# Optimization experiments

Measured on AMD Instinct MI355X. Metric: run time of the kernel, lower is better.

## Reference

```python
import jax, jax.numpy as jnp
import numpy as np
from jax import lax

# dims: batch, seq len, views, d_model; d_state, d_inner=2*d_model, d_conv, dt_rank=ceil(d_model/16)
B, L, V, D = 4, 512, 4, 256
DS, DI, DCONV, DTR = 16, 512, 4, 16
EPS = 1e-5

def setup_inputs():
    key = jax.random.key(0)
    ks = jax.random.split(key, 10)
    rn = lambda k, s, sc: jax.random.normal(k, s, jnp.float32) * sc
    return {
        "x": rn(ks[0], (B, L, V, D), 1.0),
        "ln_g": jnp.ones((V, D), jnp.float32),
        "ln_b": jnp.zeros((V, D), jnp.float32),
        "w_in": rn(ks[1], (V, 2 * DI, D), D ** -0.5),
        "conv_w": rn(ks[2], (V, DI, DCONV), DCONV ** -0.5),
        "conv_b": rn(ks[3], (V, DI), 0.02),
        "w_x": rn(ks[4], (V, DTR + 2 * DS, DI), DI ** -0.5),
        "w_dt": rn(ks[5], (V, DI, DTR), DTR ** -0.5),
        "b_dt": rn(ks[6], (V, DI), 0.02),
        "A_log": rn(ks[7], (V, DI, DS), 0.5),
        "D_skip": jnp.ones((V, DI), jnp.float32),
        "w_out": rn(ks[8], (V, D, DI), DI ** -0.5),
    }

def _layernorm(x, g, b):
    mu = x.mean(-1, keepdims=True)
    var = ((x - mu) ** 2).mean(-1, keepdims=True)
    return (x - mu) * lax.rsqrt(var + EPS) * g + b

def _mamba_view(xv, w_in, conv_w, conv_b, w_x, w_dt, b_dt, A_log, D_skip, w_out):
    # xv: (B, L, D)
    xz = jnp.einsum('bld,ed->ble', xv, w_in)            # (B, L, 2*DI)
    xi, z = xz[..., :DI], xz[..., DI:]
    # causal depthwise conv over time
    xt = jnp.moveaxis(xi, 1, 2)                          # (B, DI, L)
    xt = jnp.pad(xt, ((0, 0), (0, 0), (DCONV - 1, 0)))
    xc = lax.conv_general_dilated(xt, conv_w[:, None, :], (1,), 'VALID',
                                  feature_group_count=DI,
                                  dimension_numbers=('NCH', 'OIH', 'NCH'))
    xc = jax.nn.silu(xc + conv_b[None, :, None])
    xc = jnp.moveaxis(xc, 1, 2)                          # (B, L, DI)
    xdbl = jnp.einsum('bld,ed->ble', xc, w_x)            # (B, L, DTR+2*DS)
    dt_lo = xdbl[..., :DTR]
    Bc = xdbl[..., DTR:DTR + DS]
    Cc = xdbl[..., DTR + DS:]
    delta = jax.nn.softplus(jnp.einsum('blr,dr->bld', dt_lo, w_dt) + b_dt)
    A = -jnp.exp(A_log)                                  # (DI, DS)
    dA = jnp.exp(jnp.einsum('bld,dn->bldn', delta, A))   # discretized A
    dBu = jnp.einsum('bld,bln,bld->bldn', delta, Bc, xc) # discretized B*u

    def step(h, inp):
        dA_t, dBu_t, C_t = inp
        h = dA_t * h + dBu_t                             # (B, DI, DS)
        return h, jnp.einsum('bdn,bn->bd', h, C_t)

    h0 = jnp.zeros((B, DI, DS), xv.dtype)
    _, ys = lax.scan(step, h0, (jnp.moveaxis(dA, 1, 0), jnp.moveaxis(dBu, 1, 0), jnp.moveaxis(Cc, 1, 0)))
    y = jnp.moveaxis(ys, 0, 1) + xc * D_skip             # (B, L, DI)
    y = y * jax.nn.silu(z)
    return jnp.einsum('bld,od->blo', y, w_out)           # (B, L, D)

def _forward(x, ln_g, ln_b, w_in, conv_w, conv_b, w_x, w_dt, b_dt, A_log, D_skip, w_out):
    xv = jnp.moveaxis(x, 2, 0)                           # (V, B, L, D)
    def per_view(xv_i, g, b, wi, cw, cb, wx, wdt, bdt, al, dsk, wo):
        return _mamba_view(_layernorm(xv_i, g, b), wi, cw, cb, wx, wdt, bdt, al, dsk, wo)
    outs = jax.vmap(per_view)(xv, ln_g, ln_b, w_in, conv_w, conv_b, w_x, w_dt, b_dt, A_log, D_skip, w_out)
    return jnp.moveaxis(outs, 0, 2)                      # (B, L, V, D)

def reference(x, ln_g, ln_b, w_in, conv_w, conv_b, w_x, w_dt, b_dt, A_log, D_skip, w_out):
    # eval mode: view_mask == ones, dropout identity, gather is None -> h == agents
    agents = _forward(x, ln_g, ln_b, w_in, conv_w, conv_b, w_x, w_dt, b_dt, A_log, D_skip, w_out)
    return (agents, agents)
```

## Files before the change

### kernel.cpp

```cpp
#include <hip/hip_runtime.h>
#include <hip/hip_bf16.h>
#include <math.h>

#define B_ 4
#define L_ 512
#define V_ 4
#define D_ 256
#define DS_ 16
#define DI_ 512
#define DTR_ 16
#define ML (B_*L_)
#define NC_ 32
#define CL_ 16

#define OFF_RA   0
#define SZ_RA    ((long)V_*ML*D_)
#define OFF_XZ   (OFF_RA + SZ_RA)
#define SZ_XZ    ((long)V_*ML*2*DI_)
#define OFF_XC   (OFF_XZ + SZ_XZ)
#define SZ_XC    ((long)V_*ML*DI_)
#define OFF_XDBL (OFF_XC + SZ_XC)
#define SZ_XDBL  ((long)V_*ML*48)

typedef short short8_t __attribute__((ext_vector_type(8)));
typedef float f32x4_t  __attribute__((ext_vector_type(4)));

#define LOG2E 1.44269504088896341f
#define LN2   0.69314718055994531f

__device__ __forceinline__ float exp2_fast(float x) { return __builtin_amdgcn_exp2f(x); }
__device__ __forceinline__ float softplus_fast(float x) {
    const float t = __builtin_amdgcn_exp2f(x * LOG2E);
    const float r = __builtin_amdgcn_logf(1.f + t) * LN2;
    return x > 20.f ? x : r;
}
__device__ __forceinline__ float silu_fast(float z) {
    const float t = __builtin_amdgcn_exp2f(-LOG2E * z);
    return z * __builtin_amdgcn_rcpf(1.f + t);
}
__device__ __forceinline__ ushort f2bf(float f) {
    uint u = __float_as_uint(f);
    return (ushort)((u + 0x7fffu + ((u >> 16) & 1u)) >> 16);
}
__device__ __forceinline__ float bf2f(ushort h) { return __uint_as_float(((uint)h) << 16); }

__device__ __forceinline__ long hb_idx(int v, int b, int c, int d) {
    const long s = ((((long)b*NC_ + c)*DI_ + d) << 4);
    return (long)v*ML*(2*DI_) + (s >> 9)*(2*DI_) + (s & 511);
}

__global__ __launch_bounds__(256) void split_w(const float* __restrict__ in,
                                               ushort* __restrict__ oh,
                                               ushort* __restrict__ ol, int n4)
{
    const int i = blockIdx.x*256 + threadIdx.x;
    if (i >= n4) return;
    const float4 f = ((const float4*)in)[i];
    const ushort h0=f2bf(f.x), h1=f2bf(f.y), h2=f2bf(f.z), h3=f2bf(f.w);
    ((short4*)oh)[i] = make_short4((short)h0,(short)h1,(short)h2,(short)h3);
    ((short4*)ol)[i] = make_short4((short)f2bf(f.x-bf2f(h0)), (short)f2bf(f.y-bf2f(h1)),
                                   (short)f2bf(f.z-bf2f(h2)), (short)f2bf(f.w-bf2f(h3)));
}

__global__ __launch_bounds__(256) void ln_split(const float* __restrict__ x,
                                                const float* __restrict__ g,
                                                const float* __restrict__ bta,
                                                ushort* __restrict__ xh,
                                                ushort* __restrict__ xl)
{
    const int m = blockIdx.x;
    const int v = blockIdx.y;
    const int d = threadIdx.x;
    const float val = x[((long)m*V_ + v)*D_ + d];
    float s = val, sq = val*val;
#pragma unroll
    for (int off = 32; off >= 1; off >>= 1) {
        s  += __shfl_xor(s, off);
        sq += __shfl_xor(sq, off);
    }
    __shared__ float ws[4], wq[4];
    if ((threadIdx.x & 63) == 0) { ws[threadIdx.x >> 6] = s; wq[threadIdx.x >> 6] = sq; }
    __syncthreads();
    s  = ws[0]+ws[1]+ws[2]+ws[3];
    sq = wq[0]+wq[1]+wq[2]+wq[3];
    const float mu  = s * (1.f/D_);
    const float var = sq * (1.f/D_) - mu*mu;
    const float inv = rsqrtf(var + 1e-5f);
    const float r = (val - mu)*inv*g[v*D_+d] + bta[v*D_+d];
    const ushort h = f2bf(r);
    const long idx = ((long)v*ML + m)*D_ + d;
    xh[idx] = h;
    xl[idx] = f2bf(r - bf2f(h));
}

__global__ __launch_bounds__(256,2) void mfma_gemm_in(
    const ushort* __restrict__ Ah, const ushort* __restrict__ Al,
    const ushort* __restrict__ Bh, const ushort* __restrict__ Bl,
    float* __restrict__ C)
{
    const int v = blockIdx.z;
    const long Ao = (long)v*ML*D_;
    const long Bo = (long)v*(2*DI_)*D_;
    C += (long)v*ML*(2*DI_);
    const int bm = blockIdx.y*128, bn = blockIdx.x*128;
    __shared__ ushort sAh[128][40], sAl[128][40], sBh[128][40], sBl[128][40];
    const int tid  = threadIdx.x;
    const int lane = tid & 63, w = tid >> 6;
    const int wr = w >> 1, wc = w & 1;
    const int fm = lane & 15, fg = lane >> 4;
    const int r = tid >> 1, q0 = (tid & 1)*2;

    f32x4_t acc[4][4];
#pragma unroll
    for (int i=0;i<4;++i)
#pragma unroll
        for (int j=0;j<4;++j)
#pragma unroll
            for (int k=0;k<4;++k) acc[i][j][k]=0.f;

    const ushort* Agh = Ah + Ao + (long)(bm+r)*D_ + q0*8;
    const ushort* Agl = Al + Ao + (long)(bm+r)*D_ + q0*8;
    const ushort* Bgh = Bh + Bo + (long)(bn+r)*D_ + q0*8;
    const ushort* Bgl = Bl + Bo + (long)(bn+r)*D_ + q0*8;

    for (int k0 = 0; k0 < D_; k0 += 32) {
        const uint4 a0 = *(const uint4*)(Agh + k0);
        const uint4 a1 = *(const uint4*)(Agh + k0 + 8);
        const uint4 a2 = *(const uint4*)(Agl + k0);
        const uint4 a3 = *(const uint4*)(Agl + k0 + 8);
        const uint4 b0 = *(const uint4*)(Bgh + k0);
        const uint4 b1 = *(const uint4*)(Bgh + k0 + 8);
        const uint4 b2 = *(const uint4*)(Bgl + k0);
        const uint4 b3 = *(const uint4*)(Bgl + k0 + 8);
        __syncthreads();
        *(uint4*)&sAh[r][q0*8]   = a0;  *(uint4*)&sAh[r][q0*8+8] = a1;
        *(uint4*)&sAl[r][q0*8]   = a2;  *(uint4*)&sAl[r][q0*8+8] = a3;
        *(uint4*)&sBh[r][q0*8]   = b0;  *(uint4*)&sBh[r][q0*8+8] = b1;
        *(uint4*)&sBl[r][q0*8]   = b2;  *(uint4*)&sBl[r][q0*8+8] = b3;
        __syncthreads();
        short8_t ah[4], al[4], bh[4], bl[4];
#pragma unroll
        for (int i=0;i<4;++i) {
            ah[i] = *(const short8_t*)&sAh[wr*64 + i*16 + fm][fg*8];
            al[i] = *(const short8_t*)&sAl[wr*64 + i*16 + fm][fg*8];
            bh[i] = *(const short8_t*)&sBh[wc*64 + i*16 + fm][fg*8];
            bl[i] = *(const short8_t*)&sBl[wc*64 + i*16 + fm][fg*8];
        }
#pragma unroll
        for (int i=0;i<4;++i)
#pragma unroll
            for (int j=0;j<4;++j) {
                acc[i][j] = __builtin_amdgcn_mfma_f32_16x16x32_bf16(ah[i], bh[j], acc[i][j], 0,0,0);
                acc[i][j] = __builtin_amdgcn_mfma_f32_16x16x32_bf16(ah[i], bl[j], acc[i][j], 0,0,0);
                acc[i][j] = __builtin_amdgcn_mfma_f32_16x16x32_bf16(al[i], bh[j], acc[i][j], 0,0,0);
            }
    }
#pragma unroll
    for (int i=0;i<4;++i)
#pragma unroll
        for (int j4=0;j4<4;++j4) {
            const int row = bm + wr*64 + i*16 + fg*4 + j4;
            float* cr = C + (long)row*(2*DI_) + bn + wc*64 + fm;
#pragma unroll
            for (int j=0;j<4;++j) cr[j*16] = acc[i][j][j4];
        }
}

__global__ __launch_bounds__(256,2) void mfma_gemm_out(
    const uint* __restrict__ Apk,
    const ushort* __restrict__ Bh, const ushort* __restrict__ Bl,
    float* __restrict__ Cout)
{
    const int v = blockIdx.z;
    Apk += (long)v*ML*DI_;
    const long Bo = (long)v*D_*DI_;
    const int bm = blockIdx.y*128, bn = blockIdx.x*128;
    __shared__ ushort sAh[128][40], sAl[128][40], sBh[128][40], sBl[128][40];
    const int tid  = threadIdx.x;
    const int lane = tid & 63, w = tid >> 6;
    const int wr = w >> 1, wc = w & 1;
    const int fm = lane & 15, fg = lane >> 4;
    const int r = tid >> 1, hh = tid & 1, q0 = (tid & 1)*2;

    f32x4_t acc[4][4];
#pragma unroll
    for (int i=0;i<4;++i)
#pragma unroll
        for (int j=0;j<4;++j)
#pragma unroll
            for (int k=0;k<4;++k) acc[i][j][k]=0.f;

    const uint*   Ag  = Apk + (long)(bm+r)*DI_ + hh*16;
    const ushort* Bgh = Bh + Bo + (long)(bn+r)*DI_ + q0*8;
    const ushort* Bgl = Bl + Bo + (long)(bn+r)*DI_ + q0*8;

    for (int k0 = 0; k0 < DI_; k0 += 32) {
        const uint4 p0 = *(const uint4*)(Ag + k0);
        const uint4 p1 = *(const uint4*)(Ag + k0 + 4);
        const uint4 p2 = *(const uint4*)(Ag + k0 + 8);
        const uint4 p3 = *(const uint4*)(Ag + k0 + 12);
        const uint4 b0 = *(const uint4*)(Bgh + k0);
        const uint4 b1 = *(const uint4*)(Bgh + k0 + 8);
        const uint4 b2 = *(const uint4*)(Bgl + k0);
        const uint4 b3 = *(const uint4*)(Bgl + k0 + 8);
        __syncthreads();
        *(short4*)&sAh[r][hh*16+ 0] = make_short4((short)(p0.x&0xffff),(short)(p0.y&0xffff),(short)(p0.z&0xffff),(short)(p0.w&0xffff));
        *(short4*)&sAl[r][hh*16+ 0] = make_short4((short)(p0.x>>16),(short)(p0.y>>16),(short)(p0.z>>16),(short)(p0.w>>16));
        *(short4*)&sAh[r][hh*16+ 4] = make_short4((short)(p1.x&0xffff),(short)(p1.y&0xffff),(short)(p1.z&0xffff),(short)(p1.w&0xffff));
        *(short4*)&sAl[r][hh*16+ 4] = make_short4((short)(p1.x>>16),(short)(p1.y>>16),(short)(p1.z>>16),(short)(p1.w>>16));
        *(short4*)&sAh[r][hh*16+ 8] = make_short4((short)(p2.x&0xffff),(short)(p2.y&0xffff),(short)(p2.z&0xffff),(short)(p2.w&0xffff));
        *(short4*)&sAl[r][hh*16+ 8] = make_short4((short)(p2.x>>16),(short)(p2.y>>16),(short)(p2.z>>16),(short)(p2.w>>16));
        *(short4*)&sAh[r][hh*16+12] = make_short4((short)(p3.x&0xffff),(short)(p3.y&0xffff),(short)(p3.z&0xffff),(short)(p3.w&0xffff));
        *(short4*)&sAl[r][hh*16+12] = make_short4((short)(p3.x>>16),(short)(p3.y>>16),(short)(p3.z>>16),(short)(p3.w>>16));
        *(uint4*)&sBh[r][q0*8]   = b0;  *(uint4*)&sBh[r][q0*8+8] = b1;
        *(uint4*)&sBl[r][q0*8]   = b2;  *(uint4*)&sBl[r][q0*8+8] = b3;
        __syncthreads();
        short8_t ah[4], al[4], bh[4], bl[4];
#pragma unroll
        for (int i=0;i<4;++i) {
            ah[i] = *(const short8_t*)&sAh[wr*64 + i*16 + fm][fg*8];
            al[i] = *(const short8_t*)&sAl[wr*64 + i*16 + fm][fg*8];
            bh[i] = *(const short8_t*)&sBh[wc*64 + i*16 + fm][fg*8];
            bl[i] = *(const short8_t*)&sBl[wc*64 + i*16 + fm][fg*8];
        }
#pragma unroll
        for (int i=0;i<4;++i)
#pragma unroll
            for (int j=0;j<4;++j) {
                acc[i][j] = __builtin_amdgcn_mfma_f32_16x16x32_bf16(ah[i], bh[j], acc[i][j], 0,0,0);
                acc[i][j] = __builtin_amdgcn_mfma_f32_16x16x32_bf16(ah[i], bl[j], acc[i][j], 0,0,0);
                acc[i][j] = __builtin_amdgcn_mfma_f32_16x16x32_bf16(al[i], bh[j], acc[i][j], 0,0,0);
            }
    }
    const long TOT = (long)ML * V_ * D_;
#pragma unroll
    for (int i=0;i<4;++i)
#pragma unroll
        for (int j4=0;j4<4;++j4) {
            const int row = bm + wr*64 + i*16 + fg*4 + j4;
#pragma unroll
            for (int j=0;j<4;++j) {
                const int col = bn + wc*64 + j*16 + fm;
                const long base = ((long)row*V_ + v)*D_ + col;
                const float val = acc[i][j][j4];
                Cout[base]       = val;
                Cout[base + TOT] = val;
            }
        }
}

__global__ __launch_bounds__(512) void conv_silu(const float* __restrict__ xz,
                                                 const float* __restrict__ cw,
                                                 const float* __restrict__ cb,
                                                 float* __restrict__ xc)
{
    const int m = blockIdx.x;
    const int v = blockIdx.y;
    const int c = threadIdx.x;
    const int l = m & 511;
    const float* xzv = xz + (long)v*ML*2*DI_;
    const float4 w4 = *(const float4*)&cw[((long)v*DI_ + c)*4];
    const float w[4] = {w4.x, w4.y, w4.z, w4.w};
    float acc = cb[v*DI_ + c];
#pragma unroll
    for (int k = 0; k < 4; ++k) {
        const int lp = l - 3 + k;
        if (lp >= 0) acc = fmaf(xzv[(long)(m - 3 + k)*(2*DI_) + c], w[k], acc);
    }
    xc[((long)v*ML + m)*DI_ + c] = silu_fast(acc);
}

__global__ __launch_bounds__(256) void gemm_nt48_sk(const float* __restrict__ A,
                                                    const float* __restrict__ Bm,
                                                    float* __restrict__ P,
                                                    long sAv, long sBv)
{
    const int v = blockIdx.z;
    const int ks = blockIdx.y;
    A  += (long)v * sAv;
    Bm += (long)v * sBv;
    P  += (long)v * ((long)ML*2*DI_);
    __shared__ float As[16][68];
    __shared__ float Bs[16][48];
    const int tid = threadIdx.x;
    const int tx = tid & 15, ty = tid >> 4;
    const int bm = blockIdx.x * 64;
    const int lr = tid >> 2;
    const int lk = (tid & 3) * 4;
    const float* Ag = A + (long)(bm + lr)*DI_ + lk;
    float acc[4][3] = {};
    for (int k0 = ks*128; k0 < ks*128 + 128; k0 += 16) {
        const float4 av = *(const float4*)(Ag + k0);
        float4 bv = {0,0,0,0};
        if (tid < 192) bv = *(const float4*)(Bm + (long)(tid >> 2)*DI_ + k0 + (tid & 3)*4);
        __syncthreads();
        As[lk+0][lr]=av.x; As[lk+1][lr]=av.y; As[lk+2][lr]=av.z; As[lk+3][lr]=av.w;
        if (tid < 192) {
            const int br = tid >> 2, bk = (tid & 3)*4;
            Bs[bk+0][br]=bv.x; Bs[bk+1][br]=bv.y; Bs[bk+2][br]=bv.z; Bs[bk+3][br]=bv.w;
        }
        __syncthreads();
#pragma unroll
        for (int kk = 0; kk < 16; ++kk) {
            const float4 a = *(const float4*)&As[kk][ty*4];
            const float b0 = Bs[kk][tx*3+0], b1 = Bs[kk][tx*3+1], b2 = Bs[kk][tx*3+2];
            acc[0][0]=fmaf(a.x,b0,acc[0][0]); acc[0][1]=fmaf(a.x,b1,acc[0][1]); acc[0][2]=fmaf(a.x,b2,acc[0][2]);
            acc[1][0]=fmaf(a.y,b0,acc[1][0]); acc[1][1]=fmaf(a.y,b1,acc[1][1]); acc[1][2]=fmaf(a.y,b2,acc[1][2]);
            acc[2][0]=fmaf(a.z,b0,acc[2][0]); acc[2][1]=fmaf(a.z,b1,acc[2][1]); acc[2][2]=fmaf(a.z,b2,acc[2][2]);
            acc[3][0]=fmaf(a.w,b0,acc[3][0]); acc[3][1]=fmaf(a.w,b1,acc[3][1]); acc[3][2]=fmaf(a.w,b2,acc[3][2]);
        }
    }
#pragma unroll
    for (int i = 0; i < 4; ++i)
#pragma unroll
        for (int j = 0; j < 3; ++j)
            P[(long)(bm + ty*4 + i)*(2*DI_) + ks*48 + tx*3 + j] = acc[i][j];
}

__global__ __launch_bounds__(256) void reduce48(const float* __restrict__ xz,
                                                float* __restrict__ xdbl)
{
    const long i = (long)blockIdx.x*256 + threadIdx.x;
    if (i >= (long)V_*ML*48) return;
    const long row = i / 48; const int j = (int)(i % 48);
    const float* p = xz + row*(2*DI_);
    xdbl[i] = (p[j] + p[48+j]) + (p[96+j] + p[144+j]);
}

__global__ __launch_bounds__(256) void scanA(const float* __restrict__ xcin,
                                             const float* __restrict__ xdbl,
                                             const float* __restrict__ A_log,
                                             const float* __restrict__ wdt,
                                             const float* __restrict__ bdt,
                                             float* __restrict__ hxz,
                                             float* __restrict__ sdel)
{
    const int c = blockIdx.x >> 1, half = blockIdx.x & 1;
    const int b = blockIdx.y, v = blockIdx.z;
    const int d = half*256 + threadIdx.x;
    const long rowbase = (long)v*ML + (long)b*L_ + (long)c*CL_;
    const float* xcv = xcin + rowbase*DI_;
    const float* xdv = xdbl + rowbase*48;

    __shared__ float sX[CL_*48];
    for (int t = threadIdx.x; t < CL_*48; t += 256) sX[t] = xdv[t];

    float a2[16];
#pragma unroll
    for (int n = 0; n < 16; ++n)
        a2[n] = -exp2_fast(A_log[((long)v*DI_ + d)*DS_ + n] * LOG2E) * LOG2E;
    float wreg[16];
    {
        const float* wp = wdt + ((long)v*DI_ + d)*DTR_;
#pragma unroll
        for (int r = 0; r < 16; r += 4) {
            const float4 t4 = *(const float4*)(wp + r);
            wreg[r]=t4.x; wreg[r+1]=t4.y; wreg[r+2]=t4.z; wreg[r+3]=t4.w;
        }
    }
    const float bias = bdt[(long)v*DI_ + d];
    float h[16];
#pragma unroll
    for (int n = 0; n < 16; ++n) h[n] = 0.f;
    float sdsum = 0.f;
    __syncthreads();

    float xcur[8], xnxt[8];
#pragma unroll
    for (int s = 0; s < 8; ++s) xcur[s] = xcv[(long)s*DI_ + d];

    for (int g = 0; g < CL_; g += 8) {
        if (g + 8 < CL_) {
#pragma unroll
            for (int s = 0; s < 8; ++s) xnxt[s] = xcv[(long)(g+8+s)*DI_ + d];
        }
#pragma unroll
        for (int s = 0; s < 8; ++s) {
            const float* xrow = &sX[(g+s)*48];
            const float4 t0 = *(const float4*)&xrow[0];
            const float4 t1 = *(const float4*)&xrow[4];
            const float4 t2 = *(const float4*)&xrow[8];
            const float4 t3 = *(const float4*)&xrow[12];
            float acc = bias;
            acc = fmaf(t0.x,wreg[0],acc);  acc = fmaf(t0.y,wreg[1],acc);
            acc = fmaf(t0.z,wreg[2],acc);  acc = fmaf(t0.w,wreg[3],acc);
            acc = fmaf(t1.x,wreg[4],acc);  acc = fmaf(t1.y,wreg[5],acc);
            acc = fmaf(t1.z,wreg[6],acc);  acc = fmaf(t1.w,wreg[7],acc);
            acc = fmaf(t2.x,wreg[8],acc);  acc = fmaf(t2.y,wreg[9],acc);
            acc = fmaf(t2.z,wreg[10],acc); acc = fmaf(t2.w,wreg[11],acc);
            acc = fmaf(t3.x,wreg[12],acc); acc = fmaf(t3.y,wreg[13],acc);
            acc = fmaf(t3.z,wreg[14],acc); acc = fmaf(t3.w,wreg[15],acc);
            const float delta = softplus_fast(acc);
            const float tx = delta * xcur[s];
            sdsum += delta;
#pragma unroll
            for (int n4 = 0; n4 < 4; ++n4) {
                const float4 Bv = *(const float4*)&xrow[16 + n4*4];
                h[n4*4+0] = fmaf(exp2_fast(delta*a2[n4*4+0]), h[n4*4+0], tx*Bv.x);
                h[n4*4+1] = fmaf(exp2_fast(delta*a2[n4*4+1]), h[n4*4+1], tx*Bv.y);
                h[n4*4+2] = fmaf(exp2_fast(delta*a2[n4*4+2]), h[n4*4+2], tx*Bv.z);
                h[n4*4+3] = fmaf(exp2_fast(delta*a2[n4*4+3]), h[n4*4+3], tx*Bv.w);
            }
        }
#pragma unroll
        for (int s = 0; s < 8; ++s) xcur[s] = xnxt[s];
    }
    float* hb = hxz + hb_idx(v, b, c, d);
#pragma unroll
    for (int n = 0; n < 16; n += 4) {
        float4 r; r.x = h[n]; r.y = h[n+1]; r.z = h[n+2]; r.w = h[n+3];
        *(float4*)&hb[n] = r;
    }
    sdel[(((long)v*B_ + b)*NC_ + c)*DI_ + d] = sdsum;
}

__global__ __launch_bounds__(256) void scanB(const float* __restrict__ A_log,
                                             const float* __restrict__ sdel,
                                             float* __restrict__ hxz)
{
    const long lin = (long)blockIdx.x*256 + threadIdx.x;
    const int n = (int)(lin & 15);
    const int d = (int)((lin >> 4) & 511);
    const int b = (int)((lin >> 13) & 3);
    const int v = (int)(lin >> 15);
    const float a2 = -exp2_fast(A_log[((long)v*DI_ + d)*DS_ + n] * LOG2E) * LOG2E;
    float h = 0.f;
    long hidx = hb_idx(v, b, 0, d) + n;
    long sidx = ((long)(v*B_ + b)*NC_)*DI_ + d;
#pragma unroll
    for (int c = 0; c < NC_; ++c) {
        const float he = hxz[hidx];
        const float P  = exp2_fast(a2 * sdel[sidx]);
        hxz[hidx] = h;
        h = fmaf(P, h, he);
        hidx += (long)16*(2*DI_);
        sidx += DI_;
    }
}

__global__ __launch_bounds__(256) void scanC(const float* __restrict__ xz,
                                             const float* __restrict__ xcin,
                                             const float* __restrict__ xdbl,
                                             const float* __restrict__ A_log,
                                             const float* __restrict__ wdt,
                                             const float* __restrict__ bdt,
                                             const float* __restrict__ D_skip,
                                             float* __restrict__ yout)
{
    const int c = blockIdx.x >> 1, half = blockIdx.x & 1;
    const int b = blockIdx.y, v = blockIdx.z;
    const int d = half*256 + threadIdx.x;
    const long rowbase = (long)v*ML + (long)b*L_ + (long)c*CL_;
    const float* xzv = xz   + rowbase*(2*DI_);
    const float* xcv = xcin + rowbase*DI_;
    const float* xdv = xdbl + rowbase*48;
    uint*        yv  = (uint*)yout + rowbase*DI_;

    __shared__ float sX[CL_*48];
    for (int t = threadIdx.x; t < CL_*48; t += 256) sX[t] = xdv[t];

    float a2[16];
#pragma unroll
    for (int n = 0; n < 16; ++n)
        a2[n] = -exp2_fast(A_log[((long)v*DI_ + d)*DS_ + n] * LOG2E) * LOG2E;
    float wreg[16];
    {
        const float* wp = wdt + ((long)v*DI_ + d)*DTR_;
#pragma unroll
        for (int r = 0; r < 16; r += 4) {
            const float4 t4 = *(const float4*)(wp + r);
            wreg[r]=t4.x; wreg[r+1]=t4.y; wreg[r+2]=t4.z; wreg[r+3]=t4.w;
        }
    }
    const float bias = bdt[(long)v*DI_ + d];
    const float dsk = D_skip[v*DI_ + d];
    float h[16];
    const float* hb = xz + hb_idx(v, b, c, d);
#pragma unroll
    for (int n = 0; n < 16; n += 4) {
        const float4 r = *(const float4*)&hb[n];
        h[n] = r.x; h[n+1] = r.y; h[n+2] = r.z; h[n+3] = r.w;
    }
    __syncthreads();

    float xcur[8], zcur[8], xnxt[8], znxt[8];
#pragma unroll
    for (int s = 0; s < 8; ++s) {
        xcur[s] = xcv[(long)s*DI_ + d];
        zcur[s] = xzv[(long)s*(2*DI_) + DI_ + d];
    }

    for (int g = 0; g < CL_; g += 8) {
        if (g + 8 < CL_) {
#pragma unroll
            for (int s = 0; s < 8; ++s) {
                xnxt[s] = xcv[(long)(g+8+s)*DI_ + d];
                znxt[s] = xzv[(long)(g+8+s)*(2*DI_) + DI_ + d];
            }
        }
#pragma unroll
        for (int s = 0; s < 8; ++s) {
            const float* xrow = &sX[(g+s)*48];
            const float4 t0 = *(const float4*)&xrow[0];
            const float4 t1 = *(const float4*)&xrow[4];
            const float4 t2 = *(const float4*)&xrow[8];
            const float4 t3 = *(const float4*)&xrow[12];
            float acc = bias;
            acc = fmaf(t0.x,wreg[0],acc);  acc = fmaf(t0.y,wreg[1],acc);
            acc = fmaf(t0.z,wreg[2],acc);  acc = fmaf(t0.w,wreg[3],acc);
            acc = fmaf(t1.x,wreg[4],acc);  acc = fmaf(t1.y,wreg[5],acc);
            acc = fmaf(t1.z,wreg[6],acc);  acc = fmaf(t1.w,wreg[7],acc);
            acc = fmaf(t2.x,wreg[8],acc);  acc = fmaf(t2.y,wreg[9],acc);
            acc = fmaf(t2.z,wreg[10],acc); acc = fmaf(t2.w,wreg[11],acc);
            acc = fmaf(t3.x,wreg[12],acc); acc = fmaf(t3.y,wreg[13],acc);
            acc = fmaf(t3.z,wreg[14],acc); acc = fmaf(t3.w,wreg[15],acc);
            const float delta = softplus_fast(acc);
            const float xcval = xcur[s];
            const float tx = delta * xcval;
            float ys = 0.f;
#pragma unroll
            for (int n4 = 0; n4 < 4; ++n4) {
                const float4 Bv = *(const float4*)&xrow[16 + n4*4];
                const float4 Cv = *(const float4*)&xrow[32 + n4*4];
                h[n4*4+0] = fmaf(exp2_fast(delta*a2[n4*4+0]), h[n4*4+0], tx*Bv.x);
                h[n4*4+1] = fmaf(exp2_fast(delta*a2[n4*4+1]), h[n4*4+1], tx*Bv.y);
                h[n4*4+2] = fmaf(exp2_fast(delta*a2[n4*4+2]), h[n4*4+2], tx*Bv.z);
                h[n4*4+3] = fmaf(exp2_fast(delta*a2[n4*4+3]), h[n4*4+3], tx*Bv.w);
                ys = fmaf(h[n4*4+0], Cv.x, ys);
                ys = fmaf(h[n4*4+1], Cv.y, ys);
                ys = fmaf(h[n4*4+2], Cv.z, ys);
                ys = fmaf(h[n4*4+3], Cv.w, ys);
            }
            float outv = ys + xcval * dsk;
            outv *= silu_fast(zcur[s]);
            const ushort hv = f2bf(outv);
            const ushort lv = f2bf(outv - bf2f(hv));
            yv[(long)(g+s)*DI_ + d] = (uint)hv | ((uint)lv << 16);
        }
#pragma unroll
        for (int s = 0; s < 8; ++s) { xcur[s] = xnxt[s]; zcur[s] = znxt[s]; }
    }
}

extern "C" void kernel_launch(void* const* d_in, const int* in_sizes, int n_in,
                              void* d_out, int out_size, void* d_ws, size_t ws_size,
                              hipStream_t stream)
{
    const float* x      = (const float*)d_in[0];
    const float* ln_g   = (const float*)d_in[1];
    const float* ln_b   = (const float*)d_in[2];
    const float* w_in   = (const float*)d_in[3];
    const float* conv_w = (const float*)d_in[4];
    const float* conv_b = (const float*)d_in[5];
    const float* w_x    = (const float*)d_in[6];
    const float* w_dt   = (const float*)d_in[7];
    const float* b_dt   = (const float*)d_in[8];
    const float* A_log  = (const float*)d_in[9];
    const float* D_skip = (const float*)d_in[10];
    const float* w_out  = (const float*)d_in[11];
    float* out = (float*)d_out;

    float* ws   = (float*)d_ws;
    float* xz   = ws + OFF_XZ;
    float* xc   = ws + OFF_XC;
    float* xdbl = ws + OFF_XDBL;
    float* sdel = ws + OFF_RA;

    ushort* xlnh = (ushort*)(ws + OFF_RA);
    ushort* xlnl = xlnh + (long)V_*ML*D_;
    ushort* wih = (ushort*)(ws + OFF_XC);
    ushort* wil = wih + (long)V_*(2*DI_)*D_;
    ushort* woh = (ushort*)(ws + OFF_RA);
    ushort* wol = woh + (long)V_*D_*DI_;

    split_w<<<dim3((V_*(2*DI_)*D_/4 + 255)/256), 256, 0, stream>>>(w_in, wih, wil, V_*(2*DI_)*D_/4);

    ln_split<<<dim3(ML, V_), 256, 0, stream>>>(x, ln_g, ln_b, xlnh, xlnl);

    mfma_gemm_in<<<dim3((2*DI_)/128, ML/128, V_), 256, 0, stream>>>(xlnh, xlnl, wih, wil, xz);

    conv_silu<<<dim3(ML, V_), DI_, 0, stream>>>(xz, conv_w, conv_b, xc);

    gemm_nt48_sk<<<dim3(ML/64, 4, V_), 256, 0, stream>>>(
        xc, w_x, xz, (long)ML*DI_, (long)48*DI_);
    reduce48<<<dim3((V_*ML*48 + 255)/256), 256, 0, stream>>>(xz, xdbl);

    scanA<<<dim3(NC_*2, B_, V_), 256, 0, stream>>>(xc, xdbl, A_log, w_dt, b_dt, xz, sdel);
    scanB<<<dim3((V_*B_*DI_*DS_)/256), 256, 0, stream>>>(A_log, sdel, xz);
    scanC<<<dim3(NC_*2, B_, V_), 256, 0, stream>>>(xz, xc, xdbl, A_log, w_dt, b_dt,
                                                   D_skip, xc);

    split_w<<<dim3((V_*D_*DI_/4 + 255)/256), 256, 0, stream>>>(w_out, woh, wol, V_*D_*DI_/4);

    mfma_gemm_out<<<dim3(D_/128, ML/128, V_), 256, 0, stream>>>((const uint*)xc, woh, wol, out);
}
```

Measured before the change: 228.2 us.

## Drop LDS staging in MFMA GEMMs, fuse split-K reduction into scan, separate workspace buffers

The input and output MFMA GEMMs now load their bf16 hi/lo fragments straight from global memory into registers instead of staging them through shared memory with barriers. The output GEMM uses 64-row tiles over a separate hi/lo y layout, which doubles its grid. The standalone reduce48 kernel is removed, and scanA/scanC sum the four split-K partials while loading their shared tile. The workspace is split into dedicated, non-aliased buffers and both weight splits run up front. The aim is to cut barrier overhead, one kernel launch and a round trip through memory, at the cost of uncoalesced, non-shared global fragment loads that rely on the cache for reuse across waves.

```diff
diff --git a/kernel.cpp b/kernel.cpp
--- a/kernel.cpp
+++ b/kernel.cpp
@@ -13,14 +13,24 @@
 #define NC_ 32
 #define CL_ 16
 
-#define OFF_RA   0
-#define SZ_RA    ((long)V_*ML*D_)
-#define OFF_XZ   (OFF_RA + SZ_RA)
-#define SZ_XZ    ((long)V_*ML*2*DI_)
-#define OFF_XC   (OFF_XZ + SZ_XZ)
-#define SZ_XC    ((long)V_*ML*DI_)
-#define OFF_XDBL (OFF_XC + SZ_XC)
-#define SZ_XDBL  ((long)V_*ML*48)
+#define OFF_XZ    0L
+#define SZ_XZ     ((long)V_*ML*2*DI_)
+#define OFF_XC    (OFF_XZ + SZ_XZ)
+#define SZ_XC     ((long)V_*ML*DI_)
+#define OFF_XLN   (OFF_XC + SZ_XC)
+#define SZ_XLN    ((long)V_*ML*D_)
+#define OFF_WIN   (OFF_XLN + SZ_XLN)
+#define SZ_WIN    ((long)V_*(2*DI_)*D_)
+#define OFF_WOUT  (OFF_WIN + SZ_WIN)
+#define SZ_WOUT   ((long)V_*D_*DI_)
+#define OFF_Y     (OFF_WOUT + SZ_WOUT)
+#define SZ_Y      ((long)V_*ML*DI_)
+#define OFF_P     (OFF_Y + SZ_Y)
+#define SZ_P      ((long)V_*ML*192)
+#define OFF_HB    (OFF_P + SZ_P)
+#define SZ_HB     ((long)V_*B_*NC_*DI_*16)
+#define OFF_SDEL  (OFF_HB + SZ_HB)
+#define SZ_SDEL   ((long)V_*B_*NC_*DI_)
 
 typedef short short8_t __attribute__((ext_vector_type(8)));
 typedef float f32x4_t  __attribute__((ext_vector_type(4)));
@@ -43,11 +53,6 @@
     return (ushort)((u + 0x7fffu + ((u >> 16) & 1u)) >> 16);
 }
 __device__ __forceinline__ float bf2f(ushort h) { return __uint_as_float(((uint)h) << 16); }
-
-__device__ __forceinline__ long hb_idx(int v, int b, int c, int d) {
-    const long s = ((((long)b*NC_ + c)*DI_ + d) << 4);
-    return (long)v*ML*(2*DI_) + (s >> 9)*(2*DI_) + (s & 511);
-}
 
 __global__ __launch_bounds__(256) void split_w(const float* __restrict__ in,
                                                ushort* __restrict__ oh,
@@ -93,22 +98,19 @@
     xl[idx] = f2bf(r - bf2f(h));
 }
 
-__global__ __launch_bounds__(256,2) void mfma_gemm_in(
+__global__ __launch_bounds__(256) void mfma_gemm_in(
     const ushort* __restrict__ Ah, const ushort* __restrict__ Al,
     const ushort* __restrict__ Bh, const ushort* __restrict__ Bl,
     float* __restrict__ C)
 {
     const int v = blockIdx.z;
-    const long Ao = (long)v*ML*D_;
-    const long Bo = (long)v*(2*DI_)*D_;
-    C += (long)v*ML*(2*DI_);
     const int bm = blockIdx.y*128, bn = blockIdx.x*128;
-    __shared__ ushort sAh[128][40], sAl[128][40], sBh[128][40], sBl[128][40];
-    const int tid  = threadIdx.x;
-    const int lane = tid & 63, w = tid >> 6;
+    const int lane = threadIdx.x & 63, w = threadIdx.x >> 6;
     const int wr = w >> 1, wc = w & 1;
     const int fm = lane & 15, fg = lane >> 4;
-    const int r = tid >> 1, q0 = (tid & 1)*2;
+    const long Ab = (long)v*ML*D_       + (long)(bm + wr*64 + fm)*D_ + fg*8;
+    const long Bb = (long)v*(2*DI_)*D_  + (long)(bn + wc*64 + fm)*D_ + fg*8;
+    C += (long)v*ML*(2*DI_);
 
     f32x4_t acc[4][4];
 #pragma unroll
@@ -118,33 +120,15 @@
 #pragma unroll
             for (int k=0;k<4;++k) acc[i][j][k]=0.f;
 
-    const ushort* Agh = Ah + Ao + (long)(bm+r)*D_ + q0*8;
-    const ushort* Agl = Al + Ao + (long)(bm+r)*D_ + q0*8;
-    const ushort* Bgh = Bh + Bo + (long)(bn+r)*D_ + q0*8;
-    const ushort* Bgl = Bl + Bo + (long)(bn+r)*D_ + q0*8;
-
+#pragma unroll 2
     for (int k0 = 0; k0 < D_; k0 += 32) {
-        const uint4 a0 = *(const uint4*)(Agh + k0);
-        const uint4 a1 = *(const uint4*)(Agh + k0 + 8);
-        const uint4 a2 = *(const uint4*)(Agl + k0);
-        const uint4 a3 = *(const uint4*)(Agl + k0 + 8);
-        const uint4 b0 = *(const uint4*)(Bgh + k0);
-        const uint4 b1 = *(const uint4*)(Bgh + k0 + 8);
-        const uint4 b2 = *(const uint4*)(Bgl + k0);
-        const uint4 b3 = *(const uint4*)(Bgl + k0 + 8);
-        __syncthreads();
-        *(uint4*)&sAh[r][q0*8]   = a0;  *(uint4*)&sAh[r][q0*8+8] = a1;
-        *(uint4*)&sAl[r][q0*8]   = a2;  *(uint4*)&sAl[r][q0*8+8] = a3;
-        *(uint4*)&sBh[r][q0*8]   = b0;  *(uint4*)&sBh[r][q0*8+8] = b1;
-        *(uint4*)&sBl[r][q0*8]   = b2;  *(uint4*)&sBl[r][q0*8+8] = b3;
-        __syncthreads();
         short8_t ah[4], al[4], bh[4], bl[4];
 #pragma unroll
-        for (int i=0;i<4;++i) {
-            ah[i] = *(const short8_t*)&sAh[wr*64 + i*16 + fm][fg*8];
-            al[i] = *(const short8_t*)&sAl[wr*64 + i*16 + fm][fg*8];
-            bh[i] = *(const short8_t*)&sBh[wc*64 + i*16 + fm][fg*8];
-            bl[i] = *(const short8_t*)&sBl[wc*64 + i*16 + fm][fg*8];
+        for (int i = 0; i < 4; ++i) {
+            ah[i] = *(const short8_t*)(Ah + Ab + (long)i*16*D_ + k0);
+            al[i] = *(const short8_t*)(Al + Ab + (long)i*16*D_ + k0);
+            bh[i] = *(const short8_t*)(Bh + Bb + (long)i*16*D_ + k0);
+            bl[i] = *(const short8_t*)(Bl + Bb + (long)i*16*D_ + k0);
         }
 #pragma unroll
         for (int i=0;i<4;++i)
@@ -166,65 +150,42 @@
         }
 }
 
-__global__ __launch_bounds__(256,2) void mfma_gemm_out(
-    const uint* __restrict__ Apk,
-    const ushort* __restrict__ Bh, const ushort* __restrict__ Bl,
+__global__ __launch_bounds__(256) void mfma_gemm_out(
+    const ushort* __restrict__ Ahp, const ushort* __restrict__ Alp,
+    const ushort* __restrict__ Bh,  const ushort* __restrict__ Bl,
     float* __restrict__ Cout)
 {
     const int v = blockIdx.z;
-    Apk += (long)v*ML*DI_;
-    const long Bo = (long)v*D_*DI_;
-    const int bm = blockIdx.y*128, bn = blockIdx.x*128;
-    __shared__ ushort sAh[128][40], sAl[128][40], sBh[128][40], sBl[128][40];
-    const int tid  = threadIdx.x;
-    const int lane = tid & 63, w = tid >> 6;
+    const int bm = blockIdx.y*64, bn = blockIdx.x*128;
+    const int lane = threadIdx.x & 63, w = threadIdx.x >> 6;
     const int wr = w >> 1, wc = w & 1;
     const int fm = lane & 15, fg = lane >> 4;
-    const int r = tid >> 1, hh = tid & 1, q0 = (tid & 1)*2;
-
-    f32x4_t acc[4][4];
-#pragma unroll
-    for (int i=0;i<4;++i)
+    const long Ab = (long)v*ML*DI_ + (long)(bm + wr*32 + fm)*DI_ + fg*8;
+    const long Bb = (long)v*D_*DI_ + (long)(bn + wc*64 + fm)*DI_ + fg*8;
+
+    f32x4_t acc[2][4];
+#pragma unroll
+    for (int i=0;i<2;++i)
 #pragma unroll
         for (int j=0;j<4;++j)
 #pragma unroll
             for (int k=0;k<4;++k) acc[i][j][k]=0.f;
 
-    const uint*   Ag  = Apk + (long)(bm+r)*DI_ + hh*16;
-    const ushort* Bgh = Bh + Bo + (long)(bn+r)*DI_ + q0*8;
-    const ushort* Bgl = Bl + Bo + (long)(bn+r)*DI_ + q0*8;
-
+#pragma unroll 2
     for (int k0 = 0; k0 < DI_; k0 += 32) {
-        const uint4 p0 = *(const uint4*)(Ag + k0);
-        const uint4 p1 = *(const uint4*)(Ag + k0 + 4);
-        const uint4 p2 = *(const uint4*)(Ag + k0 + 8);
-        const uint4 p3 = *(const uint4*)(Ag + k0 + 12);
-        const uint4 b0 = *(const uint4*)(Bgh + k0);
-        const uint4 b1 = *(const uint4*)(Bgh + k0 + 8);
-        const uint4 b2 = *(const uint4*)(Bgl + k0);
-        const uint4 b3 = *(const uint4*)(Bgl + k0 + 8);
-        __syncthreads();
-        *(short4*)&sAh[r][hh*16+ 0] = make_short4((short)(p0.x&0xffff),(short)(p0.y&0xffff),(short)(p0.z&0xffff),(short)(p0.w&0xffff));
-        *(short4*)&sAl[r][hh*16+ 0] = make_short4((short)(p0.x>>16),(short)(p0.y>>16),(short)(p0.z>>16),(short)(p0.w>>16));
-        *(short4*)&sAh[r][hh*16+ 4] = make_short4((short)(p1.x&0xffff),(short)(p1.y&0xffff),(short)(p1.z&0xffff),(short)(p1.w&0xffff));
-        *(short4*)&sAl[r][hh*16+ 4] = make_short4((short)(p1.x>>16),(short)(p1.y>>16),(short)(p1.z>>16),(short)(p1.w>>16));
-        *(short4*)&sAh[r][hh*16+ 8] = make_short4((short)(p2.x&0xffff),(short)(p2.y&0xffff),(short)(p2.z&0xffff),(short)(p2.w&0xffff));
-        *(short4*)&sAl[r][hh*16+ 8] = make_short4((short)(p2.x>>16),(short)(p2.y>>16),(short)(p2.z>>16),(short)(p2.w>>16));
-        *(short4*)&sAh[r][hh*16+12] = make_short4((short)(p3.x&0xffff),(short)(p3.y&0xffff),(short)(p3.z&0xffff),(short)(p3.w&0xffff));
-        *(short4*)&sAl[r][hh*16+12] = make_short4((short)(p3.x>>16),(short)(p3.y>>16),(short)(p3.z>>16),(short)(p3.w>>16));
-        *(uint4*)&sBh[r][q0*8]   = b0;  *(uint4*)&sBh[r][q0*8+8] = b1;
-        *(uint4*)&sBl[r][q0*8]   = b2;  *(uint4*)&sBl[r][q0*8+8] = b3;
-        __syncthreads();
-        short8_t ah[4], al[4], bh[4], bl[4];
-#pragma unroll
-        for (int i=0;i<4;++i) {
-            ah[i] = *(const short8_t*)&sAh[wr*64 + i*16 + fm][fg*8];
-            al[i] = *(const short8_t*)&sAl[wr*64 + i*16 + fm][fg*8];
-            bh[i] = *(const short8_t*)&sBh[wc*64 + i*16 + fm][fg*8];
-            bl[i] = *(const short8_t*)&sBl[wc*64 + i*16 + fm][fg*8];
-        }
-#pragma unroll
-        for (int i=0;i<4;++i)
+        short8_t ah[2], al[2], bh[4], bl[4];
+#pragma unroll
+        for (int i = 0; i < 2; ++i) {
+            ah[i] = *(const short8_t*)(Ahp + Ab + (long)i*16*DI_ + k0);
+            al[i] = *(const short8_t*)(Alp + Ab + (long)i*16*DI_ + k0);
+        }
+#pragma unroll
+        for (int j = 0; j < 4; ++j) {
+            bh[j] = *(const short8_t*)(Bh + Bb + (long)j*16*DI_ + k0);
+            bl[j] = *(const short8_t*)(Bl + Bb + (long)j*16*DI_ + k0);
+        }
+#pragma unroll
+        for (int i=0;i<2;++i)
 #pragma unroll
             for (int j=0;j<4;++j) {
                 acc[i][j] = __builtin_amdgcn_mfma_f32_16x16x32_bf16(ah[i], bh[j], acc[i][j], 0,0,0);
@@ -234,10 +195,10 @@
     }
     const long TOT = (long)ML * V_ * D_;
 #pragma unroll
-    for (int i=0;i<4;++i)
+    for (int i=0;i<2;++i)
 #pragma unroll
         for (int j4=0;j4<4;++j4) {
-            const int row = bm + wr*64 + i*16 + fg*4 + j4;
+            const int row = bm + wr*32 + i*16 + fg*4 + j4;
 #pragma unroll
             for (int j=0;j<4;++j) {
                 const int col = bn + wc*64 + j*16 + fm;
@@ -272,14 +233,13 @@
 
 __global__ __launch_bounds__(256) void gemm_nt48_sk(const float* __restrict__ A,
                                                     const float* __restrict__ Bm,
-                                                    float* __restrict__ P,
-                                                    long sAv, long sBv)
+                                                    float* __restrict__ P)
 {
     const int v = blockIdx.z;
     const int ks = blockIdx.y;
-    A  += (long)v * sAv;
-    Bm += (long)v * sBv;
-    P  += (long)v * ((long)ML*2*DI_);
+    A  += (long)v * ((long)ML*DI_);
+    Bm += (long)v * ((long)48*DI_);
+    P  += (long)v * ((long)ML*192);
     __shared__ float As[16][68];
     __shared__ float Bs[16][48];
     const int tid = threadIdx.x;
@@ -314,25 +274,15 @@
     for (int i = 0; i < 4; ++i)
 #pragma unroll
         for (int j = 0; j < 3; ++j)
-            P[(long)(bm + ty*4 + i)*(2*DI_) + ks*48 + tx*3 + j] = acc[i][j];
-}
-
-__global__ __launch_bounds__(256) void reduce48(const float* __restrict__ xz,
-                                                float* __restrict__ xdbl)
-{
-    const long i = (long)blockIdx.x*256 + threadIdx.x;
-    if (i >= (long)V_*ML*48) return;
-    const long row = i / 48; const int j = (int)(i % 48);
-    const float* p = xz + row*(2*DI_);
-    xdbl[i] = (p[j] + p[48+j]) + (p[96+j] + p[144+j]);
+            P[(long)(bm + ty*4 + i)*192 + ks*48 + tx*3 + j] = acc[i][j];
 }
 
 __global__ __launch_bounds__(256) void scanA(const float* __restrict__ xcin,
-                                             const float* __restrict__ xdbl,
+                                             const float* __restrict__ part,
                                              const float* __restrict__ A_log,
                                              const float* __restrict__ wdt,
                                              const float* __restrict__ bdt,
-                                             float* __restrict__ hxz,
+                                             float* __restrict__ hbuf,
                                              float* __restrict__ sdel)
 {
     const int c = blockIdx.x >> 1, half = blockIdx.x & 1;
@@ -340,10 +290,14 @@
     const int d = half*256 + threadIdx.x;
     const long rowbase = (long)v*ML + (long)b*L_ + (long)c*CL_;
     const float* xcv = xcin + rowbase*DI_;
-    const float* xdv = xdbl + rowbase*48;
+    const float* pv  = part + rowbase*192;
 
     __shared__ float sX[CL_*48];
-    for (int t = threadIdx.x; t < CL_*48; t += 256) sX[t] = xdv[t];
+    for (int t = threadIdx.x; t < CL_*48; t += 256) {
+        const int row = t/48, j = t - row*48;
+        const float* pr = pv + (long)row*192 + j;
+        sX[t] = (pr[0] + pr[48]) + (pr[96] + pr[144]);
+    }
 
     float a2[16];
 #pragma unroll
@@ -405,7 +359,7 @@
 #pragma unroll
         for (int s = 0; s < 8; ++s) xcur[s] = xnxt[s];
     }
-    float* hb = hxz + hb_idx(v, b, c, d);
+    float* hb = hbuf + ((((long)v*B_ + b)*NC_ + c)*DI_ + d)*16;
 #pragma unroll
     for (int n = 0; n < 16; n += 4) {
         float4 r; r.x = h[n]; r.y = h[n+1]; r.z = h[n+2]; r.w = h[n+3];
@@ -416,7 +370,7 @@
 
 __global__ __launch_bounds__(256) void scanB(const float* __restrict__ A_log,
                                              const float* __restrict__ sdel,
-                                             float* __restrict__ hxz)
+                                             float* __restrict__ hbuf)
 {
     const long lin = (long)blockIdx.x*256 + threadIdx.x;
     const int n = (int)(lin & 15);
@@ -425,27 +379,29 @@
     const int v = (int)(lin >> 15);
     const float a2 = -exp2_fast(A_log[((long)v*DI_ + d)*DS_ + n] * LOG2E) * LOG2E;
     float h = 0.f;
-    long hidx = hb_idx(v, b, 0, d) + n;
+    long hidx = (((long)(v*B_ + b)*NC_)*DI_ + d)*16 + n;
     long sidx = ((long)(v*B_ + b)*NC_)*DI_ + d;
 #pragma unroll
     for (int c = 0; c < NC_; ++c) {
-        const float he = hxz[hidx];
+        const float he = hbuf[hidx];
         const float P  = exp2_fast(a2 * sdel[sidx]);
-        hxz[hidx] = h;
+        hbuf[hidx] = h;
         h = fmaf(P, h, he);
-        hidx += (long)16*(2*DI_);
+        hidx += (long)DI_*16;
         sidx += DI_;
     }
 }
 
 __global__ __launch_bounds__(256) void scanC(const float* __restrict__ xz,
                                              const float* __restrict__ xcin,
-                                             const float* __restrict__ xdbl,
+                                             const float* __restrict__ part,
                                              const float* __restrict__ A_log,
                                              const float* __restrict__ wdt,
                                              const float* __restrict__ bdt,
                                              const float* __restrict__ D_skip,
-                                             float* __restrict__ yout)
+                                             const float* __restrict__ hbuf,
+                                             ushort* __restrict__ yh,
+                                             ushort* __restrict__ yl)
 {
     const int c = blockIdx.x >> 1, half = blockIdx.x & 1;
     const int b = blockIdx.y, v = blockIdx.z;
@@ -453,11 +409,16 @@
     const long rowbase = (long)v*ML + (long)b*L_ + (long)c*CL_;
     const float* xzv = xz   + rowbase*(2*DI_);
     const float* xcv = xcin + rowbase*DI_;
-    const float* xdv = xdbl + rowbase*48;
-    uint*        yv  = (uint*)yout + rowbase*DI_;
+    const float* pv  = part + rowbase*192;
+    ushort* yhv = yh + rowbase*DI_;
+    ushort* ylv = yl + rowbase*DI_;
 
     __shared__ float sX[CL_*48];
-    for (int t = threadIdx.x; t < CL_*48; t += 256) sX[t] = xdv[t];
+    for (int t = threadIdx.x; t < CL_*48; t += 256) {
+        const int row = t/48, j = t - row*48;
+        const float* pr = pv + (long)row*192 + j;
+        sX[t] = (pr[0] + pr[48]) + (pr[96] + pr[144]);
+    }
 
     float a2[16];
 #pragma unroll
@@ -475,7 +436,7 @@
     const float bias = bdt[(long)v*DI_ + d];
     const float dsk = D_skip[v*DI_ + d];
     float h[16];
-    const float* hb = xz + hb_idx(v, b, c, d);
+    const float* hb = hbuf + ((((long)v*B_ + b)*NC_ + c)*DI_ + d)*16;
 #pragma unroll
     for (int n = 0; n < 16; n += 4) {
         const float4 r = *(const float4*)&hb[n];
@@ -535,7 +496,8 @@
             outv *= silu_fast(zcur[s]);
             const ushort hv = f2bf(outv);
             const ushort lv = f2bf(outv - bf2f(hv));
-            yv[(long)(g+s)*DI_ + d] = (uint)hv | ((uint)lv << 16);
+            yhv[(long)(g+s)*DI_ + d] = hv;
+            ylv[(long)(g+s)*DI_ + d] = lv;
         }
 #pragma unroll
         for (int s = 0; s < 8; ++s) { xcur[s] = xnxt[s]; zcur[s] = znxt[s]; }
@@ -563,17 +525,21 @@
     float* ws   = (float*)d_ws;
     float* xz   = ws + OFF_XZ;
     float* xc   = ws + OFF_XC;
-    float* xdbl = ws + OFF_XDBL;
-    float* sdel = ws + OFF_RA;
-
-    ushort* xlnh = (ushort*)(ws + OFF_RA);
+    float* pbuf = ws + OFF_P;
+    float* hbuf = ws + OFF_HB;
+    float* sdel = ws + OFF_SDEL;
+
+    ushort* xlnh = (ushort*)(ws + OFF_XLN);
     ushort* xlnl = xlnh + (long)V_*ML*D_;
-    ushort* wih = (ushort*)(ws + OFF_XC);
-    ushort* wil = wih + (long)V_*(2*DI_)*D_;
-    ushort* woh = (ushort*)(ws + OFF_RA);
-    ushort* wol = woh + (long)V_*D_*DI_;
+    ushort* wih  = (ushort*)(ws + OFF_WIN);
+    ushort* wil  = wih + (long)V_*(2*DI_)*D_;
+    ushort* woh  = (ushort*)(ws + OFF_WOUT);
+    ushort* wol  = woh + (long)V_*D_*DI_;
+    ushort* yh   = (ushort*)(ws + OFF_Y);
+    ushort* yl   = yh + (long)V_*ML*DI_;
 
     split_w<<<dim3((V_*(2*DI_)*D_/4 + 255)/256), 256, 0, stream>>>(w_in, wih, wil, V_*(2*DI_)*D_/4);
+    split_w<<<dim3((V_*D_*DI_/4 + 255)/256), 256, 0, stream>>>(w_out, woh, wol, V_*D_*DI_/4);
 
     ln_split<<<dim3(ML, V_), 256, 0, stream>>>(x, ln_g, ln_b, xlnh, xlnl);
 
@@ -581,16 +547,12 @@
 
     conv_silu<<<dim3(ML, V_), DI_, 0, stream>>>(xz, conv_w, conv_b, xc);
 
-    gemm_nt48_sk<<<dim3(ML/64, 4, V_), 256, 0, stream>>>(
-        xc, w_x, xz, (long)ML*DI_, (long)48*DI_);
-    reduce48<<<dim3((V_*ML*48 + 255)/256), 256, 0, stream>>>(xz, xdbl);
-
-    scanA<<<dim3(NC_*2, B_, V_), 256, 0, stream>>>(xc, xdbl, A_log, w_dt, b_dt, xz, sdel);
-    scanB<<<dim3((V_*B_*DI_*DS_)/256), 256, 0, stream>>>(A_log, sdel, xz);
-    scanC<<<dim3(NC_*2, B_, V_), 256, 0, stream>>>(xz, xc, xdbl, A_log, w_dt, b_dt,
-                                                   D_skip, xc);
-
-    split_w<<<dim3((V_*D_*DI_/4 + 255)/256), 256, 0, stream>>>(w_out, woh, wol, V_*D_*DI_/4);
-
-    mfma_gemm_out<<<dim3(D_/128, ML/128, V_), 256, 0, stream>>>((const uint*)xc, woh, wol, out);
-}
+    gemm_nt48_sk<<<dim3(ML/64, 4, V_), 256, 0, stream>>>(xc, w_x, pbuf);
+
+    scanA<<<dim3(NC_*2, B_, V_), 256, 0, stream>>>(xc, pbuf, A_log, w_dt, b_dt, hbuf, sdel);
+    scanB<<<dim3((V_*B_*DI_*DS_)/256), 256, 0, stream>>>(A_log, sdel, hbuf);
+    scanC<<<dim3(NC_*2, B_, V_), 256, 0, stream>>>(xz, xc, pbuf, A_log, w_dt, b_dt,
+                                                   D_skip, hbuf, yh, yl);
+
+    mfma_gemm_out<<<dim3(D_/128, ML/64, V_), 256, 0, stream>>>(yh, yl, woh, wol, out);
+}
```

After: 238.1 us. 1.04x slower.
